# Optimization experiments

Measured on AMD Instinct MI355X. Metric: run time of the kernel, lower is better.

The kernel has to match this reference:

```python
import jax, jax.numpy as jnp
import numpy as np

B, T, BEL, S, A, HID, EI, ES = 512, 50, 1024, 256, 32, 1024, 1024, 256
MIN_STD = 0.1


def _lin(key, out_d, in_d):
    # torch nn.Linear default init: U(-1/sqrt(fan_in), 1/sqrt(fan_in))
    k1, k2 = jax.random.split(key)
    s = 1.0 / np.sqrt(in_d)
    W = jax.random.uniform(k1, (out_d, in_d), minval=-s, maxval=s, dtype=jnp.float32)
    b = jax.random.uniform(k2, (out_d,), minval=-s, maxval=s, dtype=jnp.float32)
    return W, b


def setup_inputs() -> dict:
    key = jax.random.key(0)
    ks = jax.random.split(key, 16)
    inp = {
        'prev_state': jax.random.normal(ks[0], (B, S), jnp.float32),
        'actions': jax.random.normal(ks[1], (T, B, A), jnp.float32),
        'prev_belief': jax.random.normal(ks[2], (B, BEL), jnp.float32),
        'obs_image': jax.random.normal(ks[3], (T, B, EI), jnp.float32),
        'obs_sound': jax.random.normal(ks[4], (T, B, ES), jnp.float32),
        'nonterminals': jnp.ones((T, B, 1), jnp.float32),
    }
    inp['W_emb'], inp['b_emb'] = _lin(ks[5], BEL, S + A)
    inp['W_ih'], inp['b_ih'] = _lin(ks[6], 3 * BEL, BEL)
    inp['W_hh'], inp['b_hh'] = _lin(ks[7], 3 * BEL, BEL)
    inp['W_s1'], inp['b_s1'] = _lin(ks[8], HID, BEL)
    inp['W_s2'], inp['b_s2'] = _lin(ks[9], 2 * S, HID)
    inp['W_ei1'], inp['b_ei1'] = _lin(ks[10], HID, BEL + EI)
    inp['W_ei2'], inp['b_ei2'] = _lin(ks[11], 2 * S, HID)
    inp['W_es1'], inp['b_es1'] = _lin(ks[12], HID, BEL + ES)
    inp['W_es2'], inp['b_es2'] = _lin(ks[13], 2 * S, HID)
    return inp


def _gru(x, h, W_ih, W_hh, b_ih, b_hh):
    gi = x @ W_ih.T + b_ih
    gh = h @ W_hh.T + b_hh
    i_r, i_z, i_n = jnp.split(gi, 3, axis=-1)
    h_r, h_z, h_n = jnp.split(gh, 3, axis=-1)
    r = jax.nn.sigmoid(i_r + h_r)
    z = jax.nn.sigmoid(i_z + h_z)
    n = jnp.tanh(i_n + r * h_n)
    return (1.0 - z) * n + z * h


def _gauss_head(x, W1, b1, W2, b2):
    h = jax.nn.relu(x @ W1.T + b1)
    ls = h @ W2.T + b2
    loc, scale = jnp.split(ls, 2, axis=-1)
    return loc, jax.nn.softplus(scale) + MIN_STD


def _poe(locs, scales):
    # precision-weighted product of Gaussian experts over axis 0
    prec = 1.0 / (scales * scales)
    var = 1.0 / jnp.sum(prec, axis=0)
    loc = var * jnp.sum(locs * prec, axis=0)
    return loc, jnp.sqrt(var)


def reference(prev_state, actions, prev_belief, obs_image, obs_sound, nonterminals,
              W_emb, b_emb, W_ih, W_hh, b_ih, b_hh,
              W_s1, b_s1, W_s2, b_s2,
              W_ei1, b_ei1, W_ei2, b_ei2,
              W_es1, b_es1, W_es2, b_es2):
    # det=True mode: prior_states = prior_means, posterior_states = posterior_means
    def step(carry, xs):
        belief, post = carry
        a_t, nt_t, oi_t, os_t = xs
        st = post * nt_t                                   # [B,S]
        hidden = jax.nn.relu(jnp.concatenate([st, a_t], axis=1) @ W_emb.T + b_emb)
        belief = _gru(hidden, belief, W_ih, W_hh, b_ih, b_hh)  # [B,BEL]
        p_loc, p_scale = _gauss_head(belief, W_s1, b_s1, W_s2, b_s2)
        i_loc, i_scale = _gauss_head(jnp.concatenate([belief, oi_t], axis=1), W_ei1, b_ei1, W_ei2, b_ei2)
        s_loc, s_scale = _gauss_head(jnp.concatenate([belief, os_t], axis=1), W_es1, b_es1, W_es2, b_es2)
        # PoE fusion with unit-Gaussian prior expert
        locs = jnp.stack([jnp.zeros_like(i_loc), i_loc, s_loc], axis=0)
        scales = jnp.stack([jnp.ones_like(i_scale), i_scale, s_scale], axis=0)
        q_loc, q_scale = _poe(locs, scales)
        new_post = q_loc  # det
        out = (belief, p_loc, p_loc, p_scale, new_post, q_loc, q_scale)
        return (belief, new_post), out

    (_, _), outs = jax.lax.scan(step, (prev_belief, prev_state),
                                (actions, nonterminals, obs_image, obs_sound))
    beliefs, prior_states, prior_means, prior_std_devs, post_states, post_means, post_std_devs = outs
    return (beliefs, prior_states, prior_means, prior_std_devs,
            post_states, post_means, post_std_devs)
```

## Files before the change

### kernel.cpp

```cpp
#include <hip/hip_runtime.h>
#include <stdint.h>

static const int T_ = 50;
static const int B_ = 512;
static const int BEL = 1024;
static const int S_ = 256;
static const int A_ = 32;
static const int EI_ = 1024;
static const int ES_ = 256;

typedef __attribute__((ext_vector_type(8))) short bf16x8;
typedef __attribute__((ext_vector_type(4))) float f32x4;

__device__ __forceinline__ short f2bf(float f) {
  union { float f; uint32_t u; } cv; cv.f = f;
  uint32_t u = cv.u;
  u = (u + 0x7fffu + ((u >> 16) & 1u)) >> 16;
  return (short)u;
}
__device__ __forceinline__ float bf2f(short s) {
  union { uint32_t u; float f; } cv;
  cv.u = ((uint32_t)(uint16_t)s) << 16;
  return cv.f;
}
__device__ __forceinline__ float softplusf(float x) {
  return (x > 20.f) ? x : log1pf(expf(x));
}

#define SZ_BEL_ALL (50ull * 512ull * 1024ull)
#define SZ_TBS     (50ull * 512ull * 256ull)
#define OFF_PS  (SZ_BEL_ALL)
#define OFF_PM  (OFF_PS + SZ_TBS)
#define OFF_PSD (OFF_PM + SZ_TBS)
#define OFF_QS  (OFF_PSD + SZ_TBS)
#define OFF_QM  (OFF_QS + SZ_TBS)
#define OFF_QSD (OFF_QM + SZ_TBS)

__global__ void k_convert(const float* __restrict__ src, short* __restrict__ dst, int n) {
  int i = (blockIdx.x * blockDim.x + threadIdx.x) * 4;
  if (i >= n) return;
  float4 v = *(const float4*)(src + i);
  short4 o;
  o.x = f2bf(v.x); o.y = f2bf(v.y); o.z = f2bf(v.z); o.w = f2bf(v.w);
  *(short4*)(dst + i) = o;
}

__global__ void k_init(const float* __restrict__ prev_belief, const float* __restrict__ prev_state,
                       const float* __restrict__ nt0,
                       float* __restrict__ belief_f32, short* __restrict__ belief_bf,
                       short* __restrict__ st_bf) {
  int i = blockIdx.x * blockDim.x + threadIdx.x;
  if (i < B_ * BEL) {
    float v = prev_belief[i];
    belief_f32[i] = v;
    belief_bf[i] = f2bf(v);
  } else {
    int k = i - B_ * BEL;
    if (k < B_ * S_) {
      int b = k / S_;
      st_bf[k] = f2bf(prev_state[k] * nt0[b]);
    }
  }
}

__global__ void k_gru(const float* __restrict__ gi, const float* __restrict__ gh,
                      const float* __restrict__ b_ih, const float* __restrict__ b_hh,
                      float* __restrict__ belief_f32, short* __restrict__ belief_bf,
                      float* __restrict__ out_beliefs_t) {
  int i = blockIdx.x * blockDim.x + threadIdx.x;
  if (i >= B_ * BEL) return;
  int b = i / BEL, j = i % BEL;
  size_t base = (size_t)b * 3 * BEL;
  float ir = gi[base + j]            + b_ih[j];
  float iz = gi[base + BEL + j]      + b_ih[BEL + j];
  float in_ = gi[base + 2 * BEL + j] + b_ih[2 * BEL + j];
  float hr = gh[base + j]            + b_hh[j];
  float hz = gh[base + BEL + j]      + b_hh[BEL + j];
  float hn = gh[base + 2 * BEL + j]  + b_hh[2 * BEL + j];
  float rr = 1.f / (1.f + expf(-(ir + hr)));
  float zz = 1.f / (1.f + expf(-(iz + hz)));
  float nn = tanhf(in_ + rr * hn);
  float h = belief_f32[i];
  float hnew = (1.f - zz) * nn + zz * h;
  belief_f32[i] = hnew;
  out_beliefs_t[i] = hnew;
  belief_bf[i] = f2bf(hnew);
}

__global__ void k_post(const float* __restrict__ ls_p, const float* __restrict__ ls_i,
                       const float* __restrict__ ls_s, const float* __restrict__ nt_next,
                       short* __restrict__ st_bf, float* __restrict__ out, int t) {
  int i = blockIdx.x * blockDim.x + threadIdx.x;
  if (i >= B_ * S_) return;
  int b = i / S_, j = i % S_;
  size_t r2 = (size_t)b * 2 * S_;
  float pl  = ls_p[r2 + j];
  float psc = softplusf(ls_p[r2 + S_ + j]) + 0.1f;
  float il  = ls_i[r2 + j];
  float isc = softplusf(ls_i[r2 + S_ + j]) + 0.1f;
  float sl  = ls_s[r2 + j];
  float ssc = softplusf(ls_s[r2 + S_ + j]) + 0.1f;
  float pi = 1.f / (isc * isc);
  float ps = 1.f / (ssc * ssc);
  float var = 1.f / (1.f + pi + ps);
  float ql = var * (il * pi + sl * ps);
  float qs = sqrtf(var);
  size_t tb = (size_t)t * B_ * S_ + i;
  out[OFF_PS + tb]  = pl;
  out[OFF_PM + tb]  = pl;
  out[OFF_PSD + tb] = psc;
  out[OFF_QS + tb]  = ql;
  out[OFF_QM + tb]  = ql;
  out[OFF_QSD + tb] = qs;
  if (nt_next) st_bf[i] = f2bf(ql * nt_next[b]);
}

struct Job {
  const short* A;
  int lda;
  const short* W;
  int ldw;
  const float* bias;
  const short* Cadd;
  float* outF;
  short* outB;
  int K;
  int relu;
};
struct Jobs { Job j[3]; };

template <int BM, int BN>
__global__ __launch_bounds__(256) void k_gemm(Jobs jobs, int N) {
  Job jb = jobs.j[blockIdx.z];
  const int tid = threadIdx.x;
  const int wave = tid >> 6;
  const int lane = tid & 63;
  const int quad = lane >> 4;
  const int r16 = lane & 15;
  const int mBase = blockIdx.y * BM;
  const int nBase = blockIdx.x * BN;
  const int K = jb.K;
  const int lda = jb.lda;
  const int ldw = jb.ldw;

  __shared__ short As[BM * 32];
  __shared__ short Bs[BN * 32];

  constexpr int WM = BM / 2, WN = BN / 2;
  constexpr int TM = WM / 16, TN = WN / 16;
  const int waveM = (wave >> 1) * WM;
  const int waveN = (wave & 1) * WN;

  f32x4 acc[TM][TN];
#pragma unroll
  for (int a = 0; a < TM; ++a)
#pragma unroll
    for (int b = 0; b < TN; ++b)
      acc[a][b] = (f32x4){0.f, 0.f, 0.f, 0.f};

  const short* Aptr = jb.A + (size_t)mBase * lda;
  const short* Wptr = jb.W + (size_t)nBase * ldw;
  const int srow = tid >> 2;
  const int scol = (tid & 3) * 8;

  for (int k0 = 0; k0 < K; k0 += 32) {
    __syncthreads();
#pragma unroll
    for (int c = 0; c < BM / 64; ++c) {
      const short* g = Aptr + (size_t)(c * 64 + srow) * lda + k0 + scol;
      __builtin_amdgcn_global_load_lds(
          (const __attribute__((address_space(1))) void*)g,
          (__attribute__((address_space(3))) void*)(&As[c * 2048 + wave * 512]), 16, 0, 0);
    }
#pragma unroll
    for (int c = 0; c < BN / 64; ++c) {
      const short* g = Wptr + (size_t)(c * 64 + srow) * ldw + k0 + scol;
      __builtin_amdgcn_global_load_lds(
          (const __attribute__((address_space(1))) void*)g,
          (__attribute__((address_space(3))) void*)(&Bs[c * 2048 + wave * 512]), 16, 0, 0);
    }
    __syncthreads();

    bf16x8 af[TM], bfr[TN];
#pragma unroll
    for (int mi = 0; mi < TM; ++mi)
      af[mi] = *(const bf16x8*)(&As[(waveM + mi * 16 + r16) * 32 + quad * 8]);
#pragma unroll
    for (int ni = 0; ni < TN; ++ni)
      bfr[ni] = *(const bf16x8*)(&Bs[(waveN + ni * 16 + r16) * 32 + quad * 8]);
#pragma unroll
    for (int mi = 0; mi < TM; ++mi)
#pragma unroll
      for (int ni = 0; ni < TN; ++ni)
        acc[mi][ni] = __builtin_amdgcn_mfma_f32_16x16x32_bf16(af[mi], bfr[ni], acc[mi][ni], 0, 0, 0);
  }

#pragma unroll
  for (int mi = 0; mi < TM; ++mi) {
#pragma unroll
    for (int ni = 0; ni < TN; ++ni) {
#pragma unroll
      for (int reg = 0; reg < 4; ++reg) {
        int row = mBase + waveM + mi * 16 + quad * 4 + reg;
        int col = nBase + waveN + ni * 16 + r16;
        float v = acc[mi][ni][reg];
        if (jb.bias) v += jb.bias[col];
        if (jb.Cadd) v += bf2f(jb.Cadd[(size_t)row * N + col]);
        if (jb.relu) v = v > 0.f ? v : 0.f;
        if (jb.outF) jb.outF[(size_t)row * N + col] = v;
        if (jb.outB) jb.outB[(size_t)row * N + col] = f2bf(v);
      }
    }
  }
}

extern "C" void kernel_launch(void* const* d_in, const int* in_sizes, int n_in,
                              void* d_out, int out_size, void* d_ws, size_t ws_size,
                              hipStream_t stream) {
  const float* prev_state  = (const float*)d_in[0];
  const float* actions     = (const float*)d_in[1];
  const float* prev_belief = (const float*)d_in[2];
  const float* obs_image   = (const float*)d_in[3];
  const float* obs_sound   = (const float*)d_in[4];
  const float* nonterm     = (const float*)d_in[5];
  const float* W_emb = (const float*)d_in[6];  const float* b_emb = (const float*)d_in[7];
  const float* W_ih  = (const float*)d_in[8];  const float* b_ih  = (const float*)d_in[9];
  const float* W_hh  = (const float*)d_in[10]; const float* b_hh  = (const float*)d_in[11];
  const float* W_s1  = (const float*)d_in[12]; const float* b_s1  = (const float*)d_in[13];
  const float* W_s2  = (const float*)d_in[14]; const float* b_s2  = (const float*)d_in[15];
  const float* W_ei1 = (const float*)d_in[16]; const float* b_ei1 = (const float*)d_in[17];
  const float* W_ei2 = (const float*)d_in[18]; const float* b_ei2 = (const float*)d_in[19];
  const float* W_es1 = (const float*)d_in[20]; const float* b_es1 = (const float*)d_in[21];
  const float* W_es2 = (const float*)d_in[22]; const float* b_es2 = (const float*)d_in[23];
  float* out = (float*)d_out;

  char* base = (char*)d_ws;
  size_t off = 0;
  auto alloc = [&](size_t bytes) -> void* {
    void* p = base + off;
    off += (bytes + 255) & ~(size_t)255;
    return p;
  };

  const size_t TB = (size_t)T_ * B_;

  short* Wemb_b = (short*)alloc((size_t)1024 * 288 * 2);
  short* Wih_b  = (short*)alloc((size_t)3072 * 1024 * 2);
  short* Whh_b  = (short*)alloc((size_t)3072 * 1024 * 2);
  short* Ws1_b  = (short*)alloc((size_t)1024 * 1024 * 2);
  short* Ws2_b  = (short*)alloc((size_t)512 * 1024 * 2);
  short* Wei1_b = (short*)alloc((size_t)1024 * 2048 * 2);
  short* Wei2_b = (short*)alloc((size_t)512 * 1024 * 2);
  short* Wes1_b = (short*)alloc((size_t)1024 * 1280 * 2);
  short* Wes2_b = (short*)alloc((size_t)512 * 1024 * 2);
  short* oi_bf  = (short*)alloc(TB * EI_ * 2);
  short* os_bf  = (short*)alloc(TB * ES_ * 2);
  short* act_bf = (short*)alloc(TB * A_ * 2);
  short* OI_c   = (short*)alloc(TB * 1024 * 2);
  short* OS_c   = (short*)alloc(TB * 1024 * 2);
  short* ACT_c  = (short*)alloc(TB * 1024 * 2);
  float* belief_f32 = (float*)alloc((size_t)B_ * BEL * 4);
  short* belief_bf  = (short*)alloc((size_t)B_ * BEL * 2);
  short* st_bf      = (short*)alloc((size_t)B_ * S_ * 2);
  short* hidden_b   = (short*)alloc((size_t)B_ * 1024 * 2);
  float* gi_f       = (float*)alloc((size_t)B_ * 3072 * 4);
  float* gh_f       = (float*)alloc((size_t)B_ * 3072 * 4);
  short* eih_b      = (short*)alloc((size_t)B_ * 1024 * 2);
  short* esh_b      = (short*)alloc((size_t)B_ * 1024 * 2);
  short* sh_b       = (short*)alloc((size_t)B_ * 1024 * 2);
  float* lsi_f      = (float*)alloc((size_t)B_ * 512 * 4);
  float* lss_f      = (float*)alloc((size_t)B_ * 512 * 4);
  float* lsp_f      = (float*)alloc((size_t)B_ * 512 * 4);

  struct Conv { const float* s; short* d; size_t n; };
  Conv convs[12] = {
      {W_emb, Wemb_b, 1024 * 288}, {W_ih, Wih_b, 3072 * 1024}, {W_hh, Whh_b, 3072 * 1024},
      {W_s1, Ws1_b, 1024 * 1024},  {W_s2, Ws2_b, 512 * 1024},  {W_ei1, Wei1_b, 1024 * 2048},
      {W_ei2, Wei2_b, 512 * 1024}, {W_es1, Wes1_b, 1024 * 1280}, {W_es2, Wes2_b, 512 * 1024},
      {obs_image, oi_bf, TB * EI_}, {obs_sound, os_bf, TB * ES_}, {actions, act_bf, TB * A_}};
  for (int c = 0; c < 12; ++c) {
    int blocks = (int)((convs[c].n / 4 + 255) / 256);
    k_convert<<<dim3(blocks), dim3(256), 0, stream>>>(convs[c].s, convs[c].d, (int)convs[c].n);
  }

  {
    Jobs jb{};
    jb.j[0] = Job{oi_bf, 1024, Wei1_b + 1024, 2048, b_ei1, nullptr, nullptr, OI_c, 1024, 0};
    jb.j[1] = jb.j[0]; jb.j[2] = jb.j[0];
    k_gemm<128, 128><<<dim3(8, 200, 1), dim3(256), 0, stream>>>(jb, 1024);
  }
  {
    Jobs jb{};
    jb.j[0] = Job{os_bf, 256, Wes1_b + 1024, 1280, b_es1, nullptr, nullptr, OS_c, 256, 0};
    jb.j[1] = jb.j[0]; jb.j[2] = jb.j[0];
    k_gemm<128, 128><<<dim3(8, 200, 1), dim3(256), 0, stream>>>(jb, 1024);
  }
  {
    Jobs jb{};
    jb.j[0] = Job{act_bf, 32, Wemb_b + 256, 288, b_emb, nullptr, nullptr, ACT_c, 32, 0};
    jb.j[1] = jb.j[0]; jb.j[2] = jb.j[0];
    k_gemm<128, 128><<<dim3(8, 200, 1), dim3(256), 0, stream>>>(jb, 1024);
  }

  k_init<<<dim3((B_ * BEL + B_ * S_) / 256), dim3(256), 0, stream>>>(
      prev_belief, prev_state, nonterm, belief_f32, belief_bf, st_bf);

  for (int t = 0; t < T_; ++t) {
    {
      Jobs jb{};
      jb.j[0] = Job{st_bf, 256, Wemb_b, 288, nullptr, ACT_c + (size_t)t * B_ * 1024,
                    nullptr, hidden_b, 256, 1};
      jb.j[1] = jb.j[0]; jb.j[2] = jb.j[0];
      k_gemm<64, 64><<<dim3(16, 8, 1), dim3(256), 0, stream>>>(jb, 1024);
    }
    {
      Jobs jb{};
      jb.j[0] = Job{hidden_b, 1024, Wih_b, 1024, nullptr, nullptr, gi_f, nullptr, 1024, 0};
      jb.j[1] = Job{belief_bf, 1024, Whh_b, 1024, nullptr, nullptr, gh_f, nullptr, 1024, 0};
      jb.j[2] = jb.j[0];
      k_gemm<128, 64><<<dim3(48, 4, 2), dim3(256), 0, stream>>>(jb, 3072);
    }
    k_gru<<<dim3(2048), dim3(256), 0, stream>>>(gi_f, gh_f, b_ih, b_hh,
                                                belief_f32, belief_bf,
                                                out + (size_t)t * B_ * BEL);
    {
      Jobs jb{};
      jb.j[0] = Job{belief_bf, 1024, Wei1_b, 2048, nullptr, OI_c + (size_t)t * B_ * 1024,
                    nullptr, eih_b, 1024, 1};
      jb.j[1] = Job{belief_bf, 1024, Wes1_b, 1280, nullptr, OS_c + (size_t)t * B_ * 1024,
                    nullptr, esh_b, 1024, 1};
      jb.j[2] = Job{belief_bf, 1024, Ws1_b, 1024, b_s1, nullptr, nullptr, sh_b, 1024, 1};
      k_gemm<128, 64><<<dim3(16, 4, 3), dim3(256), 0, stream>>>(jb, 1024);
    }
    {
      Jobs jb{};
      jb.j[0] = Job{eih_b, 1024, Wei2_b, 1024, b_ei2, nullptr, lsi_f, nullptr, 1024, 0};
      jb.j[1] = Job{esh_b, 1024, Wes2_b, 1024, b_es2, nullptr, lss_f, nullptr, 1024, 0};
      jb.j[2] = Job{sh_b, 1024, Ws2_b, 1024, b_s2, nullptr, lsp_f, nullptr, 1024, 0};
      k_gemm<64, 64><<<dim3(8, 8, 3), dim3(256), 0, stream>>>(jb, 512);
    }
    const float* ntn = (t + 1 < T_) ? (nonterm + (size_t)(t + 1) * B_) : nullptr;
    k_post<<<dim3(512), dim3(256), 0, stream>>>(lsp_f, lsi_f, lss_f, ntn, st_bf, out, t);
  }
}
```

Baseline: 5.320 ms.

## Fuse GRU gates into GEMM, fuse PoE head, hoist prior head out of loop

Adds a fused kernel that computes both GRU gate GEMMs and applies the GRU nonlinearity in the epilogue, so the fp32 gi/gh intermediates are no longer written and read back. Another kernel fuses the second-layer image and sound heads with the softplus and PoE computation. The prior head depends only on beliefs, so it is taken off the sequential path and run as two large batched GEMMs over all timesteps after the loop, followed by a vectorized elementwise kernel. The generic GEMM also gets LDS double-buffering. In exchange it stores every timestep's bf16 beliefs and reuses the OI/OS buffers as scratch once the loop ends, and the per-step fused kernels launch small grids of 256 and 64 blocks.

```diff
diff --git a/kernel.cpp b/kernel.cpp
--- a/kernel.cpp
+++ b/kernel.cpp
@@ -26,6 +26,11 @@
 __device__ __forceinline__ float softplusf(float x) {
   return (x > 20.f) ? x : log1pf(expf(x));
 }
+
+#define GLL16(gp, lp)                                                        \
+  __builtin_amdgcn_global_load_lds(                                          \
+      (const __attribute__((address_space(1))) void*)(gp),                   \
+      (__attribute__((address_space(3))) void*)(lp), 16, 0, 0)
 
 #define SZ_BEL_ALL (50ull * 512ull * 1024ull)
 #define SZ_TBS     (50ull * 512ull * 256ull)
@@ -47,13 +52,10 @@
 
 __global__ void k_init(const float* __restrict__ prev_belief, const float* __restrict__ prev_state,
                        const float* __restrict__ nt0,
-                       float* __restrict__ belief_f32, short* __restrict__ belief_bf,
-                       short* __restrict__ st_bf) {
+                       short* __restrict__ belief0_bf, short* __restrict__ st_bf) {
   int i = blockIdx.x * blockDim.x + threadIdx.x;
   if (i < B_ * BEL) {
-    float v = prev_belief[i];
-    belief_f32[i] = v;
-    belief_bf[i] = f2bf(v);
+    belief0_bf[i] = f2bf(prev_belief[i]);
   } else {
     int k = i - B_ * BEL;
     if (k < B_ * S_) {
@@ -63,56 +65,22 @@
   }
 }
 
-__global__ void k_gru(const float* __restrict__ gi, const float* __restrict__ gh,
-                      const float* __restrict__ b_ih, const float* __restrict__ b_hh,
-                      float* __restrict__ belief_f32, short* __restrict__ belief_bf,
-                      float* __restrict__ out_beliefs_t) {
+__global__ void k_prior_post(const float* __restrict__ lsp, float* __restrict__ out) {
   int i = blockIdx.x * blockDim.x + threadIdx.x;
-  if (i >= B_ * BEL) return;
-  int b = i / BEL, j = i % BEL;
-  size_t base = (size_t)b * 3 * BEL;
-  float ir = gi[base + j]            + b_ih[j];
-  float iz = gi[base + BEL + j]      + b_ih[BEL + j];
-  float in_ = gi[base + 2 * BEL + j] + b_ih[2 * BEL + j];
-  float hr = gh[base + j]            + b_hh[j];
-  float hz = gh[base + BEL + j]      + b_hh[BEL + j];
-  float hn = gh[base + 2 * BEL + j]  + b_hh[2 * BEL + j];
-  float rr = 1.f / (1.f + expf(-(ir + hr)));
-  float zz = 1.f / (1.f + expf(-(iz + hz)));
-  float nn = tanhf(in_ + rr * hn);
-  float h = belief_f32[i];
-  float hnew = (1.f - zz) * nn + zz * h;
-  belief_f32[i] = hnew;
-  out_beliefs_t[i] = hnew;
-  belief_bf[i] = f2bf(hnew);
-}
-
-__global__ void k_post(const float* __restrict__ ls_p, const float* __restrict__ ls_i,
-                       const float* __restrict__ ls_s, const float* __restrict__ nt_next,
-                       short* __restrict__ st_bf, float* __restrict__ out, int t) {
-  int i = blockIdx.x * blockDim.x + threadIdx.x;
-  if (i >= B_ * S_) return;
-  int b = i / S_, j = i % S_;
-  size_t r2 = (size_t)b * 2 * S_;
-  float pl  = ls_p[r2 + j];
-  float psc = softplusf(ls_p[r2 + S_ + j]) + 0.1f;
-  float il  = ls_i[r2 + j];
-  float isc = softplusf(ls_i[r2 + S_ + j]) + 0.1f;
-  float sl  = ls_s[r2 + j];
-  float ssc = softplusf(ls_s[r2 + S_ + j]) + 0.1f;
-  float pi = 1.f / (isc * isc);
-  float ps = 1.f / (ssc * ssc);
-  float var = 1.f / (1.f + pi + ps);
-  float ql = var * (il * pi + sl * ps);
-  float qs = sqrtf(var);
-  size_t tb = (size_t)t * B_ * S_ + i;
-  out[OFF_PS + tb]  = pl;
-  out[OFF_PM + tb]  = pl;
-  out[OFF_PSD + tb] = psc;
-  out[OFF_QS + tb]  = ql;
-  out[OFF_QM + tb]  = ql;
-  out[OFF_QSD + tb] = qs;
-  if (nt_next) st_bf[i] = f2bf(ql * nt_next[b]);
+  int r = i >> 6;
+  int j4 = (i & 63) * 4;
+  if (r >= T_ * B_) return;
+  float4 loc = *(const float4*)(lsp + (size_t)r * 512 + j4);
+  float4 sc  = *(const float4*)(lsp + (size_t)r * 512 + 256 + j4);
+  float4 psd;
+  psd.x = softplusf(sc.x) + 0.1f;
+  psd.y = softplusf(sc.y) + 0.1f;
+  psd.z = softplusf(sc.z) + 0.1f;
+  psd.w = softplusf(sc.w) + 0.1f;
+  size_t tb = (size_t)r * 256 + j4;
+  *(float4*)(out + OFF_PS + tb)  = loc;
+  *(float4*)(out + OFF_PM + tb)  = loc;
+  *(float4*)(out + OFF_PSD + tb) = psd;
 }
 
 struct Job {
@@ -143,8 +111,8 @@
   const int lda = jb.lda;
   const int ldw = jb.ldw;
 
-  __shared__ short As[BM * 32];
-  __shared__ short Bs[BN * 32];
+  __shared__ short As[2][BM * 32];
+  __shared__ short Bs[2][BN * 32];
 
   constexpr int WM = BM / 2, WN = BN / 2;
   constexpr int TM = WM / 16, TN = WN / 16;
@@ -163,36 +131,41 @@
   const int srow = tid >> 2;
   const int scol = (tid & 3) * 8;
 
-  for (int k0 = 0; k0 < K; k0 += 32) {
-    __syncthreads();
+  auto stage = [&](int buf, int k0) {
 #pragma unroll
     for (int c = 0; c < BM / 64; ++c) {
       const short* g = Aptr + (size_t)(c * 64 + srow) * lda + k0 + scol;
-      __builtin_amdgcn_global_load_lds(
-          (const __attribute__((address_space(1))) void*)g,
-          (__attribute__((address_space(3))) void*)(&As[c * 2048 + wave * 512]), 16, 0, 0);
+      GLL16(g, &As[buf][c * 2048 + wave * 512]);
     }
 #pragma unroll
     for (int c = 0; c < BN / 64; ++c) {
       const short* g = Wptr + (size_t)(c * 64 + srow) * ldw + k0 + scol;
-      __builtin_amdgcn_global_load_lds(
-          (const __attribute__((address_space(1))) void*)g,
-          (__attribute__((address_space(3))) void*)(&Bs[c * 2048 + wave * 512]), 16, 0, 0);
-    }
-    __syncthreads();
+      GLL16(g, &Bs[buf][c * 2048 + wave * 512]);
+    }
+  };
+
+  const int nk = K >> 5;
+  stage(0, 0);
+  __syncthreads();
+
+  for (int kt = 0; kt < nk; ++kt) {
+    const int cur = kt & 1;
+    if (kt + 1 < nk) stage(cur ^ 1, (kt + 1) << 5);
 
     bf16x8 af[TM], bfr[TN];
 #pragma unroll
     for (int mi = 0; mi < TM; ++mi)
-      af[mi] = *(const bf16x8*)(&As[(waveM + mi * 16 + r16) * 32 + quad * 8]);
+      af[mi] = *(const bf16x8*)(&As[cur][(waveM + mi * 16 + r16) * 32 + quad * 8]);
 #pragma unroll
     for (int ni = 0; ni < TN; ++ni)
-      bfr[ni] = *(const bf16x8*)(&Bs[(waveN + ni * 16 + r16) * 32 + quad * 8]);
+      bfr[ni] = *(const bf16x8*)(&Bs[cur][(waveN + ni * 16 + r16) * 32 + quad * 8]);
 #pragma unroll
     for (int mi = 0; mi < TM; ++mi)
 #pragma unroll
       for (int ni = 0; ni < TN; ++ni)
         acc[mi][ni] = __builtin_amdgcn_mfma_f32_16x16x32_bf16(af[mi], bfr[ni], acc[mi][ni], 0, 0, 0);
+
+    if (kt + 1 < nk) __syncthreads();
   }
 
 #pragma unroll
@@ -210,6 +183,211 @@
         if (jb.outF) jb.outF[(size_t)row * N + col] = v;
         if (jb.outB) jb.outB[(size_t)row * N + col] = f2bf(v);
       }
+    }
+  }
+}
+
+__global__ __launch_bounds__(256) void k_gates_gru(
+    const short* __restrict__ hidden,
+    const short* __restrict__ belief_old,
+    const short* __restrict__ Wih,
+    const short* __restrict__ Whh,
+    const float* __restrict__ b_ih, const float* __restrict__ b_hh,
+    const float* __restrict__ h_old,
+    float* __restrict__ beliefs_out,
+    short* __restrict__ belief_bf_new) {
+  const int tid = threadIdx.x;
+  const int wave = tid >> 6;
+  const int lane = tid & 63;
+  const int quad = lane >> 4;
+  const int r16 = lane & 15;
+  const int nBase = blockIdx.x * 32;
+  const int mBase = blockIdx.y * 64;
+  const int waveM = (wave >> 1) * 32;
+  const int waveN = (wave & 1) * 16;
+
+  __shared__ short Ah[2][64 * 32];
+  __shared__ short Ab[2][64 * 32];
+  __shared__ short Wt[2][6][32 * 32];
+
+  f32x4 acc[6][2];
+#pragma unroll
+  for (int g = 0; g < 6; ++g)
+#pragma unroll
+    for (int mi = 0; mi < 2; ++mi)
+      acc[g][mi] = (f32x4){0.f, 0.f, 0.f, 0.f};
+
+  const int srow = tid >> 2;
+  const int scol = (tid & 3) * 8;
+  const int wrow = (tid & 127) >> 2;
+  const int wsel = tid >> 7;
+
+  auto stage = [&](int buf, int k0) {
+    GLL16(hidden + (size_t)(mBase + srow) * 1024 + k0 + scol, &Ah[buf][wave * 512]);
+    GLL16(belief_old + (size_t)(mBase + srow) * 1024 + k0 + scol, &Ab[buf][wave * 512]);
+#pragma unroll
+    for (int p = 0; p < 3; ++p) {
+      const int gidx = 2 * p + wsel;
+      const short* Wsrc = (gidx < 3) ? Wih : Whh;
+      const int gofs = (gidx % 3) * 1024;
+      GLL16(Wsrc + (size_t)(nBase + gofs + wrow) * 1024 + k0 + scol,
+            &Wt[buf][gidx][(wave & 1) * 512]);
+    }
+  };
+
+  stage(0, 0);
+  __syncthreads();
+
+  for (int kt = 0; kt < 32; ++kt) {
+    const int cur = kt & 1;
+    if (kt + 1 < 32) stage(cur ^ 1, (kt + 1) << 5);
+
+    bf16x8 ah[2], ab[2], wf[6];
+#pragma unroll
+    for (int mi = 0; mi < 2; ++mi) {
+      ah[mi] = *(const bf16x8*)(&Ah[cur][(waveM + mi * 16 + r16) * 32 + quad * 8]);
+      ab[mi] = *(const bf16x8*)(&Ab[cur][(waveM + mi * 16 + r16) * 32 + quad * 8]);
+    }
+#pragma unroll
+    for (int g = 0; g < 6; ++g)
+      wf[g] = *(const bf16x8*)(&Wt[cur][g][(waveN + r16) * 32 + quad * 8]);
+
+#pragma unroll
+    for (int g = 0; g < 3; ++g)
+#pragma unroll
+      for (int mi = 0; mi < 2; ++mi)
+        acc[g][mi] = __builtin_amdgcn_mfma_f32_16x16x32_bf16(ah[mi], wf[g], acc[g][mi], 0, 0, 0);
+#pragma unroll
+    for (int g = 0; g < 3; ++g)
+#pragma unroll
+      for (int mi = 0; mi < 2; ++mi)
+        acc[3 + g][mi] = __builtin_amdgcn_mfma_f32_16x16x32_bf16(ab[mi], wf[3 + g], acc[3 + g][mi], 0, 0, 0);
+
+    if (kt + 1 < 32) __syncthreads();
+  }
+
+  const int col = nBase + waveN + r16;
+  const float bir = b_ih[col], biz = b_ih[1024 + col], bin_ = b_ih[2048 + col];
+  const float bhr = b_hh[col], bhz = b_hh[1024 + col], bhn = b_hh[2048 + col];
+#pragma unroll
+  for (int mi = 0; mi < 2; ++mi) {
+#pragma unroll
+    for (int reg = 0; reg < 4; ++reg) {
+      int row = mBase + waveM + mi * 16 + quad * 4 + reg;
+      float ir = acc[0][mi][reg] + bir;
+      float iz = acc[1][mi][reg] + biz;
+      float in_ = acc[2][mi][reg] + bin_;
+      float hr = acc[3][mi][reg] + bhr;
+      float hz = acc[4][mi][reg] + bhz;
+      float hn = acc[5][mi][reg] + bhn;
+      float rr = 1.f / (1.f + expf(-(ir + hr)));
+      float zz = 1.f / (1.f + expf(-(iz + hz)));
+      float nn = tanhf(in_ + rr * hn);
+      float h = h_old[(size_t)row * 1024 + col];
+      float hnew = (1.f - zz) * nn + zz * h;
+      beliefs_out[(size_t)row * 1024 + col] = hnew;
+      belief_bf_new[(size_t)row * 1024 + col] = f2bf(hnew);
+    }
+  }
+}
+
+__global__ __launch_bounds__(256) void k_heads2_poe(
+    const short* __restrict__ eih,
+    const short* __restrict__ esh,
+    const short* __restrict__ Wei2,
+    const short* __restrict__ Wes2,
+    const float* __restrict__ b_ei2, const float* __restrict__ b_es2,
+    const float* __restrict__ nt_next,
+    short* __restrict__ st_bf, float* __restrict__ out, int t) {
+  const int tid = threadIdx.x;
+  const int wave = tid >> 6;
+  const int lane = tid & 63;
+  const int quad = lane >> 4;
+  const int r16 = lane & 15;
+  const int jBase = blockIdx.x * 32;
+  const int mBase = blockIdx.y * 64;
+  const int waveM = (wave >> 1) * 32;
+  const int waveJ = (wave & 1) * 16;
+
+  __shared__ short Ai[2][64 * 32];
+  __shared__ short An[2][64 * 32];
+  __shared__ short Wp[2][4][32 * 32];
+
+  f32x4 acc[4][2];
+#pragma unroll
+  for (int g = 0; g < 4; ++g)
+#pragma unroll
+    for (int mi = 0; mi < 2; ++mi)
+      acc[g][mi] = (f32x4){0.f, 0.f, 0.f, 0.f};
+
+  const int srow = tid >> 2;
+  const int scol = (tid & 3) * 8;
+  const int wrow = (tid & 127) >> 2;
+  const int wsel = tid >> 7;
+
+  auto stage = [&](int buf, int k0) {
+    GLL16(eih + (size_t)(mBase + srow) * 1024 + k0 + scol, &Ai[buf][wave * 512]);
+    GLL16(esh + (size_t)(mBase + srow) * 1024 + k0 + scol, &An[buf][wave * 512]);
+#pragma unroll
+    for (int p = 0; p < 2; ++p) {
+      const int gidx = 2 * p + wsel;
+      const short* Wsrc = (gidx < 2) ? Wei2 : Wes2;
+      const int rofs = (gidx & 1) * 256;
+      GLL16(Wsrc + (size_t)(rofs + jBase + wrow) * 1024 + k0 + scol,
+            &Wp[buf][gidx][(wave & 1) * 512]);
+    }
+  };
+
+  stage(0, 0);
+  __syncthreads();
+
+  for (int kt = 0; kt < 32; ++kt) {
+    const int cur = kt & 1;
+    if (kt + 1 < 32) stage(cur ^ 1, (kt + 1) << 5);
+
+    bf16x8 ai[2], an[2], wf[4];
+#pragma unroll
+    for (int mi = 0; mi < 2; ++mi) {
+      ai[mi] = *(const bf16x8*)(&Ai[cur][(waveM + mi * 16 + r16) * 32 + quad * 8]);
+      an[mi] = *(const bf16x8*)(&An[cur][(waveM + mi * 16 + r16) * 32 + quad * 8]);
+    }
+#pragma unroll
+    for (int g = 0; g < 4; ++g)
+      wf[g] = *(const bf16x8*)(&Wp[cur][g][(waveJ + r16) * 32 + quad * 8]);
+
+#pragma unroll
+    for (int mi = 0; mi < 2; ++mi) {
+      acc[0][mi] = __builtin_amdgcn_mfma_f32_16x16x32_bf16(ai[mi], wf[0], acc[0][mi], 0, 0, 0);
+      acc[1][mi] = __builtin_amdgcn_mfma_f32_16x16x32_bf16(ai[mi], wf[1], acc[1][mi], 0, 0, 0);
+      acc[2][mi] = __builtin_amdgcn_mfma_f32_16x16x32_bf16(an[mi], wf[2], acc[2][mi], 0, 0, 0);
+      acc[3][mi] = __builtin_amdgcn_mfma_f32_16x16x32_bf16(an[mi], wf[3], acc[3][mi], 0, 0, 0);
+    }
+
+    if (kt + 1 < 32) __syncthreads();
+  }
+
+  const int jcol = jBase + waveJ + r16;
+  const float bil = b_ei2[jcol], bis = b_ei2[256 + jcol];
+  const float bsl = b_es2[jcol], bss = b_es2[256 + jcol];
+#pragma unroll
+  for (int mi = 0; mi < 2; ++mi) {
+#pragma unroll
+    for (int reg = 0; reg < 4; ++reg) {
+      int row = mBase + waveM + mi * 16 + quad * 4 + reg;
+      float il = acc[0][mi][reg] + bil;
+      float isc = softplusf(acc[1][mi][reg] + bis) + 0.1f;
+      float sl = acc[2][mi][reg] + bsl;
+      float ssc = softplusf(acc[3][mi][reg] + bss) + 0.1f;
+      float pi = 1.f / (isc * isc);
+      float ps = 1.f / (ssc * ssc);
+      float var = 1.f / (1.f + pi + ps);
+      float ql = var * (il * pi + sl * ps);
+      float qs = sqrtf(var);
+      size_t tb = (size_t)t * B_ * S_ + (size_t)row * 256 + jcol;
+      out[OFF_QS + tb]  = ql;
+      out[OFF_QM + tb]  = ql;
+      out[OFF_QSD + tb] = qs;
+      if (nt_next) st_bf[(size_t)row * 256 + jcol] = f2bf(ql * nt_next[row]);
     }
   }
 }
@@ -259,18 +437,14 @@
   short* OI_c   = (short*)alloc(TB * 1024 * 2);
   short* OS_c   = (short*)alloc(TB * 1024 * 2);
   short* ACT_c  = (short*)alloc(TB * 1024 * 2);
-  float* belief_f32 = (float*)alloc((size_t)B_ * BEL * 4);
-  short* belief_bf  = (short*)alloc((size_t)B_ * BEL * 2);
+  short* beliefs_bf = (short*)alloc(TB * BEL * 2);
+  short* belief0_bf = (short*)alloc((size_t)B_ * BEL * 2);
   short* st_bf      = (short*)alloc((size_t)B_ * S_ * 2);
   short* hidden_b   = (short*)alloc((size_t)B_ * 1024 * 2);
-  float* gi_f       = (float*)alloc((size_t)B_ * 3072 * 4);
-  float* gh_f       = (float*)alloc((size_t)B_ * 3072 * 4);
   short* eih_b      = (short*)alloc((size_t)B_ * 1024 * 2);
   short* esh_b      = (short*)alloc((size_t)B_ * 1024 * 2);
-  short* sh_b       = (short*)alloc((size_t)B_ * 1024 * 2);
-  float* lsi_f      = (float*)alloc((size_t)B_ * 512 * 4);
-  float* lss_f      = (float*)alloc((size_t)B_ * 512 * 4);
-  float* lsp_f      = (float*)alloc((size_t)B_ * 512 * 4);
+  short* sh_all  = OS_c;
+  float* lsp_all = (float*)OI_c;
 
   struct Conv { const float* s; short* d; size_t n; };
   Conv convs[12] = {
@@ -303,9 +477,13 @@
   }
 
   k_init<<<dim3((B_ * BEL + B_ * S_) / 256), dim3(256), 0, stream>>>(
-      prev_belief, prev_state, nonterm, belief_f32, belief_bf, st_bf);
-
+      prev_belief, prev_state, nonterm, belief0_bf, st_bf);
+
+  const short* belief_prev_bf = belief0_bf;
+  const float* h_prev = prev_belief;
   for (int t = 0; t < T_; ++t) {
+    short* belief_t_bf = beliefs_bf + (size_t)t * B_ * BEL;
+    float* belief_t_f  = out + (size_t)t * B_ * BEL;
     {
       Jobs jb{};
       jb.j[0] = Job{st_bf, 256, Wemb_b, 288, nullptr, ACT_c + (size_t)t * B_ * 1024,
@@ -313,33 +491,36 @@
       jb.j[1] = jb.j[0]; jb.j[2] = jb.j[0];
       k_gemm<64, 64><<<dim3(16, 8, 1), dim3(256), 0, stream>>>(jb, 1024);
     }
+    k_gates_gru<<<dim3(32, 8), dim3(256), 0, stream>>>(
+        hidden_b, belief_prev_bf, Wih_b, Whh_b, b_ih, b_hh,
+        h_prev, belief_t_f, belief_t_bf);
     {
       Jobs jb{};
-      jb.j[0] = Job{hidden_b, 1024, Wih_b, 1024, nullptr, nullptr, gi_f, nullptr, 1024, 0};
-      jb.j[1] = Job{belief_bf, 1024, Whh_b, 1024, nullptr, nullptr, gh_f, nullptr, 1024, 0};
+      jb.j[0] = Job{belief_t_bf, 1024, Wei1_b, 2048, nullptr, OI_c + (size_t)t * B_ * 1024,
+                    nullptr, eih_b, 1024, 1};
+      jb.j[1] = Job{belief_t_bf, 1024, Wes1_b, 1280, nullptr, OS_c + (size_t)t * B_ * 1024,
+                    nullptr, esh_b, 1024, 1};
       jb.j[2] = jb.j[0];
-      k_gemm<128, 64><<<dim3(48, 4, 2), dim3(256), 0, stream>>>(jb, 3072);
-    }
-    k_gru<<<dim3(2048), dim3(256), 0, stream>>>(gi_f, gh_f, b_ih, b_hh,
-                                                belief_f32, belief_bf,
-                                                out + (size_t)t * B_ * BEL);
-    {
-      Jobs jb{};
-      jb.j[0] = Job{belief_bf, 1024, Wei1_b, 2048, nullptr, OI_c + (size_t)t * B_ * 1024,
-                    nullptr, eih_b, 1024, 1};
-      jb.j[1] = Job{belief_bf, 1024, Wes1_b, 1280, nullptr, OS_c + (size_t)t * B_ * 1024,
-                    nullptr, esh_b, 1024, 1};
-      jb.j[2] = Job{belief_bf, 1024, Ws1_b, 1024, b_s1, nullptr, nullptr, sh_b, 1024, 1};
-      k_gemm<128, 64><<<dim3(16, 4, 3), dim3(256), 0, stream>>>(jb, 1024);
-    }
-    {
-      Jobs jb{};
-      jb.j[0] = Job{eih_b, 1024, Wei2_b, 1024, b_ei2, nullptr, lsi_f, nullptr, 1024, 0};
-      jb.j[1] = Job{esh_b, 1024, Wes2_b, 1024, b_es2, nullptr, lss_f, nullptr, 1024, 0};
-      jb.j[2] = Job{sh_b, 1024, Ws2_b, 1024, b_s2, nullptr, lsp_f, nullptr, 1024, 0};
-      k_gemm<64, 64><<<dim3(8, 8, 3), dim3(256), 0, stream>>>(jb, 512);
+      k_gemm<64, 64><<<dim3(16, 8, 2), dim3(256), 0, stream>>>(jb, 1024);
     }
     const float* ntn = (t + 1 < T_) ? (nonterm + (size_t)(t + 1) * B_) : nullptr;
-    k_post<<<dim3(512), dim3(256), 0, stream>>>(lsp_f, lsi_f, lss_f, ntn, st_bf, out, t);
-  }
-}
+    k_heads2_poe<<<dim3(8, 8), dim3(256), 0, stream>>>(
+        eih_b, esh_b, Wei2_b, Wes2_b, b_ei2, b_es2, ntn, st_bf, out, t);
+    belief_prev_bf = belief_t_bf;
+    h_prev = belief_t_f;
+  }
+
+  {
+    Jobs jb{};
+    jb.j[0] = Job{beliefs_bf, 1024, Ws1_b, 1024, b_s1, nullptr, nullptr, sh_all, 1024, 1};
+    jb.j[1] = jb.j[0]; jb.j[2] = jb.j[0];
+    k_gemm<128, 128><<<dim3(8, 200, 1), dim3(256), 0, stream>>>(jb, 1024);
+  }
+  {
+    Jobs jb{};
+    jb.j[0] = Job{sh_all, 1024, Ws2_b, 1024, b_s2, nullptr, lsp_all, nullptr, 1024, 0};
+    jb.j[1] = jb.j[0]; jb.j[2] = jb.j[0];
+    k_gemm<128, 128><<<dim3(4, 200, 1), dim3(256), 0, stream>>>(jb, 512);
+  }
+  k_prior_post<<<dim3(6400), dim3(256), 0, stream>>>(lsp_all, out);
+}
```

Result: no change. 5.216 ms (-2.0%).
